# Performance work log

Hardware: AMD Instinct MI355X
Metric: run time of the kernel (lower is better)

Reference implementation:

```python
import jax, jax.numpy as jnp
import numpy as np

D_MODEL = 1024
NUM_HEADS = 16
D_K = D_MODEL // NUM_HEADS


def setup_inputs() -> dict:
    key = jax.random.key(0)
    ks = jax.random.split(key, 9)
    B, S = 4, 2048
    scale = 1.0 / np.sqrt(D_MODEL)
    x = jax.random.normal(ks[0], (B, S, D_MODEL), dtype=jnp.float32)
    Wq = jax.random.uniform(ks[1], (D_MODEL, D_MODEL), jnp.float32, -scale, scale)
    Wk = jax.random.uniform(ks[2], (D_MODEL, D_MODEL), jnp.float32, -scale, scale)
    Wv = jax.random.uniform(ks[3], (D_MODEL, D_MODEL), jnp.float32, -scale, scale)
    Wo = jax.random.uniform(ks[4], (D_MODEL, D_MODEL), jnp.float32, -scale, scale)
    bq = jax.random.uniform(ks[5], (D_MODEL,), jnp.float32, -scale, scale)
    bk = jax.random.uniform(ks[6], (D_MODEL,), jnp.float32, -scale, scale)
    bv = jax.random.uniform(ks[7], (D_MODEL,), jnp.float32, -scale, scale)
    bo = jax.random.uniform(ks[8], (D_MODEL,), jnp.float32, -scale, scale)
    return {"x": x, "Wq": Wq, "bq": bq, "Wk": Wk, "bk": bk, "Wv": Wv, "bv": bv, "Wo": Wo, "bo": bo}


def _split_heads(t, B, S):
    # (B, S, D) -> (B, H, S, d_k)
    return t.reshape(B, S, NUM_HEADS, D_K).transpose(0, 2, 1, 3)


def reference(x, Wq, bq, Wk, bk, Wv, bv, Wo, bo):
    B, S, D = x.shape
    Q = _split_heads(x @ Wq + bq, B, S)
    K = _split_heads(x @ Wk + bk, B, S)
    V = _split_heads(x @ Wv + bv, B, S)
    # scores: (B, H, S, S) — naive materialization, faithful to original
    scores = jnp.einsum('bhqd,bhkd->bhqk', Q, K) / np.sqrt(D_K)
    weights = jax.nn.softmax(scores.astype(jnp.float32), axis=-1).astype(scores.dtype)
    # dropout p=0.0 in eval mode -> identity
    attn = jnp.einsum('bhqk,bhkd->bhqd', weights, V)
    attn = attn.transpose(0, 2, 1, 3).reshape(B, S, D)
    return attn @ Wo + bo
```

## Files before the change

### kernel.cpp

```cpp
#include <hip/hip_runtime.h>
#include <hip/hip_bf16.h>
#include <stdint.h>
#include <string.h>

using u16 = unsigned short;
typedef __attribute__((ext_vector_type(8))) short short8;
typedef __attribute__((ext_vector_type(4))) float f32x4;

__device__ __forceinline__ u16 f2bf(float f) {
  union { float f; unsigned int u; } x; x.f = f;
  unsigned int u = x.u;
  return (u16)((u + 0x7fffu + ((u >> 16) & 1u)) >> 16);
}
__device__ __forceinline__ unsigned int pk_bf16(float a, float b) {
  float2 t; t.x = a; t.y = b;
  __hip_bfloat162 h = __float22bfloat162_rn(t);
  unsigned int u; memcpy(&u, &h, 4);
  return u;
}
__device__ __forceinline__ void gl_lds16(const u16* g, u16* l) {
  __builtin_amdgcn_global_load_lds((const __attribute__((address_space(1))) void*)g,
                                   (__attribute__((address_space(3))) void*)l, 16, 0, 0);
}

__device__ __forceinline__ void pl_swap(unsigned int& a, unsigned int& b) {
  auto r1 = __builtin_amdgcn_permlane32_swap(a, b, false, false);
  auto r2 = __builtin_amdgcn_permlane16_swap(r1[0], r1[1], false, false);
  a = r2[0]; b = r2[1];
}

#define SCALE_LOG2E 0.18033688011112042f

__global__ void __launch_bounds__(256) conv_x(
    const float* __restrict__ in, u16* __restrict__ out, int n4) {
  const int t = blockIdx.x * 256 + threadIdx.x;
  if (t >= n4) return;
  const float4 v = ((const float4*)in)[t];
  uint2 o;
  o.x = pk_bf16(v.x, v.y);
  o.y = pk_bf16(v.z, v.w);
  ((uint2*)out)[t] = o;
}

__global__ void __launch_bounds__(256) transpose_w(
    const float* __restrict__ W0, const float* __restrict__ W1,
    const float* __restrict__ W2, const float* __restrict__ W3,
    u16* __restrict__ Wt) {
  __shared__ alignas(16) u16 t[64][65];
  const int z = blockIdx.z;
  const float* in = (z == 0) ? W0 : (z == 1) ? W1 : (z == 2) ? W2 : W3;
  u16* out = Wt + (size_t)z * 1024 * 1024;
  const int tx = threadIdx.x & 63, ty = threadIdx.x >> 6;
  const int r0 = blockIdx.y * 64, c0 = blockIdx.x * 64;
#pragma unroll
  for (int rr = ty; rr < 64; rr += 4) t[rr][tx] = f2bf(in[(size_t)(r0 + rr) * 1024 + c0 + tx]);
  __syncthreads();
#pragma unroll
  for (int rr = ty; rr < 64; rr += 4) out[(size_t)(c0 + rr) * 1024 + r0 + tx] = t[tx][rr];
}

__device__ __forceinline__ void gemm256_core(
    const u16* __restrict__ A, const u16* __restrict__ Bt,
    u16 (*As)[16384], u16 (*Bs)[8192],
    int m0, int n0, int K, f32x4 (&acc)[4][4]) {
  const int tid = threadIdx.x;
  const int wave = tid >> 6, lane = tid & 63;
  const int quad = lane >> 4, l16 = lane & 15;
  const int wm = wave >> 1, wn = wave & 1;
  const int lr8 = lane >> 3;
  const int cbg = ((lane & 7) ^ lr8) * 8;
  const int NT = K >> 6;

  const int arow = wm * 64 + l16;
  const int brow = wn * 64 + l16;
  int kx[2];
  kx[0] = ((quad    ) ^ (l16 & 7)) * 8;
  kx[1] = ((quad + 4) ^ (l16 & 7)) * 8;

#pragma unroll
  for (int u = 0; u < 4; ++u)
    gl_lds16(A + (size_t)(m0 + u * 64 + wave * 8 + lr8) * K + cbg,
             &As[0][u * 4096 + wave * 512]);
#pragma unroll
  for (int v = 0; v < 2; ++v)
    gl_lds16(Bt + (size_t)(n0 + v * 64 + wave * 8 + lr8) * K + cbg,
             &Bs[0][v * 4096 + wave * 512]);
#pragma unroll
  for (int u = 0; u < 3; ++u)
    gl_lds16(A + (size_t)(m0 + u * 64 + wave * 8 + lr8) * K + 64 + cbg,
             &As[1][u * 4096 + wave * 512]);
  asm volatile("s_waitcnt vmcnt(3)" ::: "memory");
  __builtin_amdgcn_s_barrier();

  for (int t = 0; t < NT; ++t) {
    const int p = t & 1;
    const u16* Ap = As[p];
    const u16* Bp = Bs[p];

    short8 af[4][2], bf[2][2];
#pragma unroll
    for (int i = 0; i < 4; ++i)
#pragma unroll
      for (int ks = 0; ks < 2; ++ks)
        af[i][ks] = *(const short8*)&Ap[(arow + i * 16) * 64 + kx[ks]];
#pragma unroll
    for (int j = 0; j < 2; ++j)
#pragma unroll
      for (int ks = 0; ks < 2; ++ks)
        bf[j][ks] = *(const short8*)&Bp[(brow + j * 16) * 64 + kx[ks]];
    if (t + 1 < NT) {
      gl_lds16(A + (size_t)(m0 + 3 * 64 + wave * 8 + lr8) * K + (t + 1) * 64 + cbg,
               &As[p ^ 1][3 * 4096 + wave * 512]);
      gl_lds16(Bt + (size_t)(n0 + wave * 8 + lr8) * K + (t + 1) * 64 + cbg,
               &Bs[p ^ 1][wave * 512]);
      gl_lds16(Bt + (size_t)(n0 + 64 + wave * 8 + lr8) * K + (t + 1) * 64 + cbg,
               &Bs[p ^ 1][4096 + wave * 512]);
    }
    __builtin_amdgcn_s_barrier();
    __builtin_amdgcn_s_setprio(1);
#pragma unroll
    for (int ks = 0; ks < 2; ++ks)
#pragma unroll
      for (int i = 0; i < 4; ++i)
#pragma unroll
        for (int j = 0; j < 2; ++j)
          acc[i][j] = __builtin_amdgcn_mfma_f32_16x16x32_bf16(af[i][ks], bf[j][ks], acc[i][j], 0, 0, 0);
    __builtin_amdgcn_s_setprio(0);
    __builtin_amdgcn_s_barrier();

#pragma unroll
    for (int j = 0; j < 2; ++j)
#pragma unroll
      for (int ks = 0; ks < 2; ++ks)
        bf[j][ks] = *(const short8*)&Bp[(brow + (j + 2) * 16) * 64 + kx[ks]];
    if (t + 2 < NT) {
#pragma unroll
      for (int u = 0; u < 3; ++u)
        gl_lds16(A + (size_t)(m0 + u * 64 + wave * 8 + lr8) * K + (t + 2) * 64 + cbg,
                 &As[p][u * 4096 + wave * 512]);
    }
    __builtin_amdgcn_s_barrier();
    __builtin_amdgcn_s_setprio(1);
#pragma unroll
    for (int ks = 0; ks < 2; ++ks)
#pragma unroll
      for (int i = 0; i < 4; ++i)
#pragma unroll
        for (int j = 0; j < 2; ++j)
          acc[i][j + 2] = __builtin_amdgcn_mfma_f32_16x16x32_bf16(af[i][ks], bf[j][ks], acc[i][j + 2], 0, 0, 0);
    __builtin_amdgcn_s_setprio(0);
    if (t + 2 < NT) {
      asm volatile("s_waitcnt vmcnt(3)" ::: "memory");
    } else {
      asm volatile("s_waitcnt vmcnt(0)" ::: "memory");
    }
    __builtin_amdgcn_s_barrier();
  }
}

__global__ void __launch_bounds__(512, 2) gemm_qkv(
    const u16* __restrict__ A, const u16* __restrict__ Wt,
    const float* __restrict__ bq, const float* __restrict__ bk, const float* __restrict__ bv,
    u16* __restrict__ Qb, u16* __restrict__ Kb, u16* __restrict__ Vtb) {
  __shared__ alignas(16) u16 As[2][16384];
  __shared__ alignas(16) u16 Bs[2][8192];
  const int tsel = blockIdx.x >> 3;
  const int n0 = (blockIdx.x & 7) * 128;
  const int m0 = blockIdx.y * 256;
  const u16* Bt = Wt + (size_t)tsel * 1048576;
  const float* bias = (tsel == 0) ? bq : (tsel == 1) ? bk : bv;

  f32x4 acc[4][4];
#pragma unroll
  for (int i = 0; i < 4; ++i)
#pragma unroll
    for (int j = 0; j < 4; ++j) acc[i][j] = (f32x4){0.f, 0.f, 0.f, 0.f};

  gemm256_core(A, Bt, As, Bs, m0, n0, 1024, acc);

  const int tid = threadIdx.x;
  const int wave = tid >> 6, lane = tid & 63;
  const int quad = lane >> 4, l16 = lane & 15;
  const int wm = wave >> 1, wn = wave & 1;

  if (tsel < 2) {
    u16* C = tsel ? Kb : Qb;
    const float scl = tsel ? 1.0f : SCALE_LOG2E;
#pragma unroll
    for (int j = 0; j < 4; ++j) {
      const int n = n0 + wn * 64 + j * 16 + l16;
      const float bvf = bias[n];
      const int h = n >> 6, d = n & 63;
#pragma unroll
      for (int i = 0; i < 4; ++i) {
        const int mbase = m0 + wm * 64 + i * 16 + quad * 4;
#pragma unroll
        for (int r = 0; r < 4; ++r) {
          const int m = mbase + r;
          const int b = m >> 11, s = m & 2047;
          C[((((size_t)b * 16 + h) * 2048) + s) * 64 + d] = f2bf((acc[i][j][r] + bvf) * scl);
        }
      }
    }
  } else {
#pragma unroll
    for (int j = 0; j < 4; ++j) {
      const int n = n0 + wn * 64 + j * 16 + l16;
      const float bvf = bias[n];
      const int h = n >> 6, d = n & 63;
#pragma unroll
      for (int i = 0; i < 4; ++i) {
        const int mbase = m0 + wm * 64 + i * 16 + quad * 4;
        const int b = mbase >> 11, s = mbase & 2047;
        uint2 o;
        o.x = pk_bf16(acc[i][j][0] + bvf, acc[i][j][1] + bvf);
        o.y = pk_bf16(acc[i][j][2] + bvf, acc[i][j][3] + bvf);
        *(uint2*)&Vtb[(((size_t)b * 16 + h) * 64 + d) * 2048 + s] = o;
      }
    }
  }
}

__global__ void __launch_bounds__(512, 2) gemm_out(
    const u16* __restrict__ A, const u16* __restrict__ Bt,
    const float* __restrict__ bias, float* __restrict__ C, int N) {
  __shared__ alignas(16) u16 As[2][16384];
  __shared__ alignas(16) u16 Bs[2][8192];
  const int m0 = blockIdx.y * 256;
  const int n0 = blockIdx.x * 128;
  f32x4 acc[4][4];
#pragma unroll
  for (int i = 0; i < 4; ++i)
#pragma unroll
    for (int j = 0; j < 4; ++j) acc[i][j] = (f32x4){0.f, 0.f, 0.f, 0.f};

  gemm256_core(A, Bt, As, Bs, m0, n0, 1024, acc);

  const int tid = threadIdx.x;
  const int wave = tid >> 6, lane = tid & 63;
  const int quad = lane >> 4, l16 = lane & 15;
  const int wm = wave >> 1, wn = wave & 1;
#pragma unroll
  for (int j = 0; j < 4; ++j) {
    const int n = n0 + wn * 64 + j * 16 + l16;
    const float bvf = bias[n];
#pragma unroll
    for (int i = 0; i < 4; ++i) {
      const int mbase = m0 + wm * 64 + i * 16 + quad * 4;
#pragma unroll
      for (int r = 0; r < 4; ++r)
        C[(size_t)(mbase + r) * N + n] = acc[i][j][r] + bvf;
    }
  }
}

__global__ void __launch_bounds__(256) flash_attn(
    const u16* __restrict__ Q, const u16* __restrict__ Kp,
    const u16* __restrict__ Vt, u16* __restrict__ Aout) {
  __shared__ alignas(16) u16 Qs[128 * 64];
  __shared__ alignas(16) u16 Ks[2][64 * 64];
  __shared__ alignas(16) u16 Vs[2][64 * 64];

  const int tid = threadIdx.x;
  const int wave = tid >> 6;
  const int lane = tid & 63;
  const int quad = lane >> 4;
  const int l16 = lane & 15;

  const int i = blockIdx.x;
  const int bh = (i & 7) * 8 + (i >> 7);
  const int q0 = ((i >> 3) & 15) * 128;
  const int b = bh >> 4, h = bh & 15;

  const u16* Qg = Q + (size_t)bh * 2048 * 64;
  const u16* Kg = Kp + (size_t)bh * 2048 * 64;
  const u16* Vg = Vt + (size_t)bh * 64 * 2048;

  const int lr8 = lane >> 3;
  const int cbg = ((lane & 7) ^ lr8) * 8;

#pragma unroll
  for (int t = 0; t < 4; ++t) {
    const int c = wave * 4 + t;
    gl_lds16(Qg + (size_t)(q0 + c * 8 + lr8) * 64 + cbg, &Qs[c * 8 * 64]);
  }
  {
#pragma unroll
    for (int t = 0; t < 2; ++t) {
      const int c = wave * 2 + t;
      gl_lds16(Kg + (size_t)(c * 8 + lr8) * 64 + cbg, &Ks[0][c * 8 * 64]);
      gl_lds16(Vg + (size_t)(c * 8 + lr8) * 2048 + cbg, &Vs[0][c * 8 * 64]);
    }
  }

  f32x4 oacc[2][4];
#pragma unroll
  for (int qb = 0; qb < 2; ++qb)
#pragma unroll
    for (int t = 0; t < 4; ++t) oacc[qb][t] = (f32x4){0.f, 0.f, 0.f, 0.f};
  f32x4 lacc[2];
  lacc[0] = (f32x4){0.f, 0.f, 0.f, 0.f};
  lacc[1] = (f32x4){0.f, 0.f, 0.f, 0.f};
  const int sw = (l16 & 7) * 8;

  short8 ones;
#pragma unroll
  for (int i2 = 0; i2 < 8; ++i2) ones[i2] = (short)0x3F80;

  __syncthreads();
  short8 qf[2][2];
#pragma unroll
  for (int qb = 0; qb < 2; ++qb)
#pragma unroll
    for (int ks = 0; ks < 2; ++ks)
      qf[qb][ks] = *(const short8*)&Qs[(wave * 32 + qb * 16 + l16) * 64 + (((ks * 4 + quad) * 8) ^ sw)];

  for (int kt = 0; kt < 32; ++kt) {
    const int p = kt & 1;
    if (kt + 1 < 32) {
      const int s1 = (kt + 1) * 64;
#pragma unroll
      for (int t = 0; t < 2; ++t) {
        const int c = wave * 2 + t;
        gl_lds16(Kg + (size_t)(s1 + c * 8 + lr8) * 64 + cbg, &Ks[p ^ 1][c * 8 * 64]);
        gl_lds16(Vg + (size_t)(c * 8 + lr8) * 2048 + s1 + cbg, &Vs[p ^ 1][c * 8 * 64]);
      }
    }
    const u16* Kc = &Ks[p][0];
    const u16* Vc = &Vs[p][0];

    f32x4 sacc[2][4];
#pragma unroll
    for (int qb = 0; qb < 2; ++qb)
#pragma unroll
      for (int t = 0; t < 4; ++t) sacc[qb][t] = (f32x4){0.f, 0.f, 0.f, 0.f};
#pragma unroll
    for (int ks = 0; ks < 2; ++ks) {
#pragma unroll
      for (int t = 0; t < 4; ++t) {
        const short8 akf = *(const short8*)&Kc[(t * 16 + l16) * 64 + (((ks * 4 + quad) * 8) ^ sw)];
#pragma unroll
        for (int qb = 0; qb < 2; ++qb)
          sacc[qb][t] = __builtin_amdgcn_mfma_f32_16x16x32_bf16(akf, qf[qb][ks], sacc[qb][t], 0, 0, 0);
      }
    }

    short8 bpf[2][2];
#pragma unroll
    for (int qb = 0; qb < 2; ++qb) {
      unsigned int w[4][2];
#pragma unroll
      for (int t = 0; t < 4; ++t) {
        const float p0 = __builtin_amdgcn_exp2f(sacc[qb][t][0]);
        const float p1 = __builtin_amdgcn_exp2f(sacc[qb][t][1]);
        const float p2 = __builtin_amdgcn_exp2f(sacc[qb][t][2]);
        const float p3 = __builtin_amdgcn_exp2f(sacc[qb][t][3]);
        w[t][0] = pk_bf16(p0, p1);
        w[t][1] = pk_bf16(p2, p3);
      }
      pl_swap(w[0][0], w[1][0]);
      pl_swap(w[0][1], w[1][1]);
      pl_swap(w[2][0], w[3][0]);
      pl_swap(w[2][1], w[3][1]);
      union { short8 s8; unsigned int u[4]; } pb;
      pb.u[0] = w[0][0]; pb.u[1] = w[0][1]; pb.u[2] = w[1][0]; pb.u[3] = w[1][1];
      bpf[qb][0] = pb.s8;
      pb.u[0] = w[2][0]; pb.u[1] = w[2][1]; pb.u[2] = w[3][0]; pb.u[3] = w[3][1];
      bpf[qb][1] = pb.s8;
    }

#pragma unroll
    for (int s = 0; s < 2; ++s)
#pragma unroll
      for (int qb = 0; qb < 2; ++qb)
        lacc[qb] = __builtin_amdgcn_mfma_f32_16x16x32_bf16(ones, bpf[qb][s], lacc[qb], 0, 0, 0);

#pragma unroll
    for (int s = 0; s < 2; ++s) {
#pragma unroll
      for (int t = 0; t < 4; ++t) {
        const short8 avf = *(const short8*)&Vc[(t * 16 + l16) * 64 + (((s * 4 + quad) * 8) ^ sw)];
#pragma unroll
        for (int qb = 0; qb < 2; ++qb)
          oacc[qb][t] = __builtin_amdgcn_mfma_f32_16x16x32_bf16(avf, bpf[qb][s], oacc[qb][t], 0, 0, 0);
      }
    }

    __syncthreads();
  }

#pragma unroll
  for (int qb = 0; qb < 2; ++qb) {
    const float inv = 1.0f / lacc[qb][0];
    const int qrow = q0 + wave * 32 + qb * 16 + l16;
    const size_t base = ((size_t)b * 2048 + qrow) * 1024 + h * 64 + quad * 4;
#pragma unroll
    for (int t = 0; t < 4; ++t) {
      uint2 o;
      o.x = pk_bf16(oacc[qb][t][0] * inv, oacc[qb][t][1] * inv);
      o.y = pk_bf16(oacc[qb][t][2] * inv, oacc[qb][t][3] * inv);
      *(uint2*)&Aout[base + t * 16] = o;
    }
  }
}

extern "C" void kernel_launch(void* const* d_in, const int* in_sizes, int n_in,
                              void* d_out, int out_size, void* d_ws, size_t ws_size,
                              hipStream_t stream) {
  (void)in_sizes; (void)n_in; (void)out_size; (void)ws_size;
  const float* x  = (const float*)d_in[0];
  const float* Wq = (const float*)d_in[1];
  const float* bq = (const float*)d_in[2];
  const float* Wk = (const float*)d_in[3];
  const float* bk = (const float*)d_in[4];
  const float* Wv = (const float*)d_in[5];
  const float* bv = (const float*)d_in[6];
  const float* Wo = (const float*)d_in[7];
  const float* bo = (const float*)d_in[8];
  float* out = (float*)d_out;

  u16* ws = (u16*)d_ws;
  const size_t SZ = (size_t)4 * 16 * 2048 * 64;
  u16* xb   = ws;
  u16* Qb   = ws + SZ;
  u16* Kb   = ws + 2 * SZ;
  u16* Vtb  = ws + 3 * SZ;
  u16* Wt   = ws + 4 * SZ;
  u16* Attn = ws;

  conv_x<<<dim3(8192), dim3(256), 0, stream>>>(x, xb, 2097152);
  transpose_w<<<dim3(16, 16, 4), dim3(256), 0, stream>>>(Wq, Wk, Wv, Wo, Wt);
  gemm_qkv<<<dim3(24, 32), dim3(512), 0, stream>>>(xb, Wt, bq, bk, bv, Qb, Kb, Vtb);
  flash_attn<<<dim3(1024), dim3(256), 0, stream>>>(Qb, Kb, Vtb, Attn);
  gemm_out<<<dim3(8, 32), dim3(512), 0, stream>>>(Attn, Wt + (size_t)3 * 1048576, bo, out, 1024);
}
```

Baseline: 316.4 us.

## Load Q/K/V fragments directly from global memory, drop LDS staging and barriers

Removes the LDS double-buffered staging of K and V tiles (and the Q tile) in the flash attention kernel. Each wave now loads its MFMA operand fragments straight from global memory into registers every iteration, and the per-iteration __syncthreads goes away. This cuts LDS traffic and barrier stalls. In exchange, the four waves each fetch the same K/V tiles separately through the cache, and the global-to-LDS prefetch overlap is lost, so load latency is exposed unless the compiler schedules the loads early.

```diff
diff --git a/kernel.cpp b/kernel.cpp
--- a/kernel.cpp
+++ b/kernel.cpp
@@ -257,10 +257,6 @@
 __global__ void __launch_bounds__(256) flash_attn(
     const u16* __restrict__ Q, const u16* __restrict__ Kp,
     const u16* __restrict__ Vt, u16* __restrict__ Aout) {
-  __shared__ alignas(16) u16 Qs[128 * 64];
-  __shared__ alignas(16) u16 Ks[2][64 * 64];
-  __shared__ alignas(16) u16 Vs[2][64 * 64];
-
   const int tid = threadIdx.x;
   const int wave = tid >> 6;
   const int lane = tid & 63;
@@ -276,22 +272,12 @@
   const u16* Kg = Kp + (size_t)bh * 2048 * 64;
   const u16* Vg = Vt + (size_t)bh * 64 * 2048;
 
-  const int lr8 = lane >> 3;
-  const int cbg = ((lane & 7) ^ lr8) * 8;
-
-#pragma unroll
-  for (int t = 0; t < 4; ++t) {
-    const int c = wave * 4 + t;
-    gl_lds16(Qg + (size_t)(q0 + c * 8 + lr8) * 64 + cbg, &Qs[c * 8 * 64]);
-  }
-  {
-#pragma unroll
-    for (int t = 0; t < 2; ++t) {
-      const int c = wave * 2 + t;
-      gl_lds16(Kg + (size_t)(c * 8 + lr8) * 64 + cbg, &Ks[0][c * 8 * 64]);
-      gl_lds16(Vg + (size_t)(c * 8 + lr8) * 2048 + cbg, &Vs[0][c * 8 * 64]);
-    }
-  }
+  short8 qf[2][2];
+#pragma unroll
+  for (int qb = 0; qb < 2; ++qb)
+#pragma unroll
+    for (int ks = 0; ks < 2; ++ks)
+      qf[qb][ks] = *(const short8*)&Qg[(size_t)(q0 + wave * 32 + qb * 16 + l16) * 64 + (ks * 4 + quad) * 8];
 
   f32x4 oacc[2][4];
 #pragma unroll
@@ -301,33 +287,20 @@
   f32x4 lacc[2];
   lacc[0] = (f32x4){0.f, 0.f, 0.f, 0.f};
   lacc[1] = (f32x4){0.f, 0.f, 0.f, 0.f};
-  const int sw = (l16 & 7) * 8;
 
   short8 ones;
 #pragma unroll
   for (int i2 = 0; i2 < 8; ++i2) ones[i2] = (short)0x3F80;
 
-  __syncthreads();
-  short8 qf[2][2];
-#pragma unroll
-  for (int qb = 0; qb < 2; ++qb)
+  for (int kt = 0; kt < 32; ++kt) {
+    const int s0 = kt * 64;
+
+    short8 akf[2][4];
 #pragma unroll
     for (int ks = 0; ks < 2; ++ks)
-      qf[qb][ks] = *(const short8*)&Qs[(wave * 32 + qb * 16 + l16) * 64 + (((ks * 4 + quad) * 8) ^ sw)];
-
-  for (int kt = 0; kt < 32; ++kt) {
-    const int p = kt & 1;
-    if (kt + 1 < 32) {
-      const int s1 = (kt + 1) * 64;
-#pragma unroll
-      for (int t = 0; t < 2; ++t) {
-        const int c = wave * 2 + t;
-        gl_lds16(Kg + (size_t)(s1 + c * 8 + lr8) * 64 + cbg, &Ks[p ^ 1][c * 8 * 64]);
-        gl_lds16(Vg + (size_t)(c * 8 + lr8) * 2048 + s1 + cbg, &Vs[p ^ 1][c * 8 * 64]);
-      }
-    }
-    const u16* Kc = &Ks[p][0];
-    const u16* Vc = &Vs[p][0];
+#pragma unroll
+      for (int t = 0; t < 4; ++t)
+        akf[ks][t] = *(const short8*)&Kg[(size_t)(s0 + t * 16 + l16) * 64 + (ks * 4 + quad) * 8];
 
     f32x4 sacc[2][4];
 #pragma unroll
@@ -335,15 +308,19 @@
 #pragma unroll
       for (int t = 0; t < 4; ++t) sacc[qb][t] = (f32x4){0.f, 0.f, 0.f, 0.f};
 #pragma unroll
-    for (int ks = 0; ks < 2; ++ks) {
-#pragma unroll
-      for (int t = 0; t < 4; ++t) {
-        const short8 akf = *(const short8*)&Kc[(t * 16 + l16) * 64 + (((ks * 4 + quad) * 8) ^ sw)];
+    for (int ks = 0; ks < 2; ++ks)
+#pragma unroll
+      for (int t = 0; t < 4; ++t)
 #pragma unroll
         for (int qb = 0; qb < 2; ++qb)
-          sacc[qb][t] = __builtin_amdgcn_mfma_f32_16x16x32_bf16(akf, qf[qb][ks], sacc[qb][t], 0, 0, 0);
-      }
-    }
+          sacc[qb][t] = __builtin_amdgcn_mfma_f32_16x16x32_bf16(akf[ks][t], qf[qb][ks], sacc[qb][t], 0, 0, 0);
+
+    short8 avf[2][4];
+#pragma unroll
+    for (int s = 0; s < 2; ++s)
+#pragma unroll
+      for (int t = 0; t < 4; ++t)
+        avf[s][t] = *(const short8*)&Vg[(size_t)(t * 16 + l16) * 2048 + s0 + (s * 4 + quad) * 8];
 
     short8 bpf[2][2];
 #pragma unroll
@@ -376,17 +353,12 @@
         lacc[qb] = __builtin_amdgcn_mfma_f32_16x16x32_bf16(ones, bpf[qb][s], lacc[qb], 0, 0, 0);
 
 #pragma unroll
-    for (int s = 0; s < 2; ++s) {
-#pragma unroll
-      for (int t = 0; t < 4; ++t) {
-        const short8 avf = *(const short8*)&Vc[(t * 16 + l16) * 64 + (((s * 4 + quad) * 8) ^ sw)];
+    for (int s = 0; s < 2; ++s)
+#pragma unroll
+      for (int t = 0; t < 4; ++t)
 #pragma unroll
         for (int qb = 0; qb < 2; ++qb)
-          oacc[qb][t] = __builtin_amdgcn_mfma_f32_16x16x32_bf16(avf, bpf[qb][s], oacc[qb][t], 0, 0, 0);
-      }
-    }
-
-    __syncthreads();
+          oacc[qb][t] = __builtin_amdgcn_mfma_f32_16x16x32_bf16(avf[s][t], bpf[qb][s], oacc[qb][t], 0, 0, 0);
   }
 
 #pragma unroll
```

Measured after the change: 442.9 us. +40.0%, slower.
